# Performance work log

Measured on AMD Instinct MI355X. Metric: run time of the kernel, lower is better.

Reference implementation:

```python
import jax, jax.numpy as jnp
import numpy as np

N_NODES = 50000
N_EDGES = 800000
IN_FEATS = 256
OUT_FEATS = 32
NUM_HEADS = 8
NEG_SLOPE = 0.2


def setup_inputs() -> dict:
    key = jax.random.key(0)
    k_feat, k_src, k_dst, k_w, k_al, k_ar = jax.random.split(key, 6)
    feat = jax.random.normal(k_feat, (N_NODES, IN_FEATS), dtype=jnp.float32)
    src = jax.random.randint(k_src, (N_EDGES,), 0, N_NODES)
    dst = jax.random.randint(k_dst, (N_EDGES,), 0, N_NODES)
    # fc weight, stored as [in, H*F] so projection is feat @ W
    W = jax.random.normal(k_w, (IN_FEATS, NUM_HEADS * OUT_FEATS), dtype=jnp.float32) * 0.05
    attn_l = jax.random.normal(k_al, (NUM_HEADS, OUT_FEATS), dtype=jnp.float32) * 0.1
    attn_r = jax.random.normal(k_ar, (NUM_HEADS, OUT_FEATS), dtype=jnp.float32) * 0.1
    bias = jnp.zeros((NUM_HEADS, OUT_FEATS), dtype=jnp.float32)
    return {"feat": feat, "W": W, "attn_l": attn_l, "attn_r": attn_r,
            "bias": bias, "src": src, "dst": dst}


def reference(feat, W, attn_l, attn_r, bias, src, dst):
    N = feat.shape[0]
    H, F = attn_l.shape
    # node projection: [N, H, F]
    h = (feat @ W).reshape(N, H, F)
    # per-node attention logits (source code uses feat_src for both el and er)
    el = jnp.einsum('nhf,hf->nh', h, attn_l)  # [N, H]
    er = jnp.einsum('nhf,hf->nh', h, attn_r)  # [N, H]
    # per-edge logit: u_add_v then LeakyReLU
    e = el[src] + er[dst]                      # [E, H]
    e = jnp.where(e > 0, e, NEG_SLOPE * e)
    # edge softmax normalized over incoming edges of each dst node
    m = jax.ops.segment_max(e, dst, num_segments=N)   # [N, H], -inf for 0-deg
    ex = jnp.exp(e - m[dst])                           # [E, H]
    s = jax.ops.segment_sum(ex, dst, num_segments=N)   # [N, H]
    a = ex / s[dst]                                     # [E, H]
    # weighted scatter-sum aggregation: u_mul_e -> sum
    msg = h[src] * a[:, :, None]                        # [E, H, F]
    rst = jax.ops.segment_sum(msg, dst, num_segments=N)  # [N, H, F]
    rst = rst + bias[None, :, :]
    return rst
```

## Files before the change

kernel.cpp:

```cpp
#include <hip/hip_runtime.h>
#include <math.h>

#define NN 50000
#define NE 800000
#define IN_F 256
#define HF 256
#define NH 8
#define NEG_SLOPE 0.2f
#define CAP 64

#define GEMM_BLOCKS 782
#define EDGE_BLOCKS 3125
#define ELR_BLOCKS 12500
#define AGG_BLOCKS 3125

typedef short bf16x8 __attribute__((ext_vector_type(8)));
typedef float f32x16 __attribute__((ext_vector_type(16)));

__device__ __forceinline__ unsigned short f2bf(float x) {
    unsigned u = __float_as_uint(x);
    u += 0x7FFF + ((u >> 16) & 1);
    return (unsigned short)(u >> 16);
}
__device__ __forceinline__ float bf2f(unsigned short b) {
    return __uint_as_float(((unsigned)b) << 16);
}

__global__ void fill2_kernel(const int* __restrict__ src, const int* __restrict__ dst,
                             int* __restrict__ cnt, int* __restrict__ slots) {
    int e = blockIdx.x * 256 + threadIdx.x;
    if (e < NE) {
        int d = dst[e];
        int pos = atomicAdd(&cnt[d], 1);
        if (pos < CAP) slots[(size_t)d * CAP + pos] = src[e];
    }
}

__global__ __launch_bounds__(256) void wconv_kernel(const float* __restrict__ W,
                                                    unsigned short* __restrict__ Wb) {
    int e = blockIdx.x * 256 + threadIdx.x;
    int k = e >> 8, n = e & 255;
    float x = W[e];
    int kt = k >> 5, kk = k & 31;
    Wb[((size_t)(kt * 256 + n)) * 32 + kk] = f2bf(x);
}

__global__ __launch_bounds__(256) void gemm_kernel(const float* __restrict__ feat,
                                                   const unsigned short* __restrict__ Wb,
                                                   unsigned short* __restrict__ h, int M) {
    __shared__ __align__(16) unsigned short As_hi[2][64][40];
    __shared__ __align__(16) unsigned short As_lo[2][64][40];

    const int tid = threadIdx.x;
    const int lane = tid & 63;
    const int wid = tid >> 6;
    const int bm = blockIdx.x * 64;

    const int arow = tid >> 2;
    const int achk = tid & 3;
    const int grow = bm + arow;
    const int crow = (grow < M) ? grow : 0;
    const float* ap = feat + (size_t)crow * IN_F + achk * 8;

    f32x16 acc[2][2];
    #pragma unroll
    for (int mi = 0; mi < 2; ++mi)
        #pragma unroll
        for (int ni = 0; ni < 2; ++ni)
            #pragma unroll
            for (int r = 0; r < 16; ++r) acc[mi][ni][r] = 0.f;

    const int khalf = lane >> 5;
    const int nbase = wid * 64 + (lane & 31);

    float4 cur0 = *(const float4*)(ap);
    float4 cur1 = *(const float4*)(ap + 4);

    for (int kt = 0; kt < 8; ++kt) {
        const int buf = kt & 1;
        float4 nxt0, nxt1;
        if (kt < 7) {
            nxt0 = *(const float4*)(ap + (kt + 1) * 32);
            nxt1 = *(const float4*)(ap + (kt + 1) * 32 + 4);
        }
        bf16x8 bh[2][2];
        #pragma unroll
        for (int ksc = 0; ksc < 2; ++ksc)
            #pragma unroll
            for (int ni = 0; ni < 2; ++ni)
                bh[ksc][ni] = *(const bf16x8*)(Wb
                    + ((size_t)(kt * 256) + nbase + ni * 32) * 32
                    + (ksc * 2 + khalf) * 8);

        float xs[8] = {cur0.x, cur0.y, cur0.z, cur0.w, cur1.x, cur1.y, cur1.z, cur1.w};
        unsigned hi2[4], lo2[4];
        #pragma unroll
        for (int p = 0; p < 4; ++p) {
            unsigned short h0 = f2bf(xs[2 * p]), h1 = f2bf(xs[2 * p + 1]);
            unsigned short l0 = f2bf(xs[2 * p] - bf2f(h0));
            unsigned short l1 = f2bf(xs[2 * p + 1] - bf2f(h1));
            hi2[p] = (unsigned)h0 | ((unsigned)h1 << 16);
            lo2[p] = (unsigned)l0 | ((unsigned)l1 << 16);
        }
        *(int4*)&As_hi[buf][arow][achk * 8] = make_int4(hi2[0], hi2[1], hi2[2], hi2[3]);
        *(int4*)&As_lo[buf][arow][achk * 8] = make_int4(lo2[0], lo2[1], lo2[2], lo2[3]);
        __syncthreads();

        #pragma unroll
        for (int ksc = 0; ksc < 2; ++ksc) {
            const int kchunk = ksc * 2 + khalf;
            bf16x8 ah[2], av[2];
            #pragma unroll
            for (int mi = 0; mi < 2; ++mi) {
                int r = mi * 32 + (lane & 31);
                ah[mi] = *(const bf16x8*)&As_hi[buf][r][kchunk * 8];
                av[mi] = *(const bf16x8*)&As_lo[buf][r][kchunk * 8];
            }
            #pragma unroll
            for (int mi = 0; mi < 2; ++mi)
                #pragma unroll
                for (int ni = 0; ni < 2; ++ni) {
                    acc[mi][ni] = __builtin_amdgcn_mfma_f32_32x32x16_bf16(ah[mi], bh[ksc][ni], acc[mi][ni], 0, 0, 0);
                    acc[mi][ni] = __builtin_amdgcn_mfma_f32_32x32x16_bf16(av[mi], bh[ksc][ni], acc[mi][ni], 0, 0, 0);
                }
        }
        cur0 = nxt0;
        cur1 = nxt1;
    }

    #pragma unroll
    for (int mi = 0; mi < 2; ++mi)
        #pragma unroll
        for (int ni = 0; ni < 2; ++ni)
            #pragma unroll
            for (int r = 0; r < 16; ++r) {
                int row = mi * 32 + (r & 3) + 8 * (r >> 2) + 4 * (lane >> 5);
                int col = wid * 64 + ni * 32 + (lane & 31);
                int gr = bm + row;
                if (gr < M) h[(size_t)gr * HF + col] = f2bf(acc[mi][ni][r]);
            }
}

__global__ __launch_bounds__(256) void elr_kernel(const unsigned short* __restrict__ h,
                                                  const float* __restrict__ al,
                                                  const float* __restrict__ ar,
                                                  float* __restrict__ el,
                                                  float* __restrict__ er) {
    int node = blockIdx.x * 4 + (threadIdx.x >> 6);
    if (node >= NN) return;
    int lane = threadIdx.x & 63;
    short4 hv = *(const short4*)&h[(size_t)node * HF + lane * 4];
    float h0 = bf2f((unsigned short)hv.x), h1 = bf2f((unsigned short)hv.y);
    float h2 = bf2f((unsigned short)hv.z), h3 = bf2f((unsigned short)hv.w);
    float4 alv = *(const float4*)&al[lane * 4];
    float4 arv = *(const float4*)&ar[lane * 4];
    float pl = h0 * alv.x + h1 * alv.y + h2 * alv.z + h3 * alv.w;
    float pr = h0 * arv.x + h1 * arv.y + h2 * arv.z + h3 * arv.w;
    #pragma unroll
    for (int off = 1; off < 8; off <<= 1) {
        pl += __shfl_xor(pl, off);
        pr += __shfl_xor(pr, off);
    }
    if ((lane & 7) == 0) {
        el[node * NH + (lane >> 3)] = pl;
        er[node * NH + (lane >> 3)] = pr;
    }
}

__global__ __launch_bounds__(256) void agg_kernel(const unsigned short* __restrict__ h,
                                                  const float* __restrict__ el,
                                                  const float* __restrict__ er,
                                                  const int* __restrict__ cnt,
                                                  const int* __restrict__ slots,
                                                  const float* __restrict__ bias,
                                                  float* __restrict__ out) {
    int wv = blockIdx.x * 4 + (threadIdx.x >> 6);
    int lane = threadIdx.x & 63;
    int eg = lane >> 3;
    int fg = lane & 7;
    int e2 = (lane >> 5) & 1, e1 = (lane >> 4) & 1, e0 = (lane >> 3) & 1;
    int col = fg * 32 + eg * 4;
    float4 bv = *(const float4*)&bias[col];

    #pragma unroll 1
    for (int t = 0; t < 4; ++t) {
        int node = wv * 4 + t;
        int deg = cnt[node];
        deg = deg < CAP ? deg : CAP;
        const int* sl = slots + (size_t)node * CAP;
        float er_mine = er[(size_t)node * NH + fg];

        float ssum = 0.f;
        float acc[32];
        #pragma unroll
        for (int j = 0; j < 32; ++j) acc[j] = 0.f;

        for (int i0 = 0; i0 < deg; i0 += 16) {
            int idxA = i0 + eg;
            int idxB = i0 + 8 + eg;
            bool vA = idxA < deg, vB = idxB < deg;
            int sA = sl[vA ? idxA : 0];
            int sB = sl[vB ? idxB : 0];
            float eA = el[(size_t)sA * NH + fg] + er_mine;
            float eB = el[(size_t)sB * NH + fg] + er_mine;
            eA = eA > 0.f ? eA : NEG_SLOPE * eA;
            eB = eB > 0.f ? eB : NEG_SLOPE * eB;
            float pA = vA ? __expf(eA) : 0.f;
            float pB = vB ? __expf(eB) : 0.f;
            ssum += pA + pB;
            const unsigned short* hpA = h + (size_t)sA * HF + fg * 32;
            const unsigned short* hpB = h + (size_t)sB * HF + fg * 32;
            bf16x8 va[4], vb[4];
            #pragma unroll
            for (int c = 0; c < 4; ++c) { va[c] = *(const bf16x8*)(hpA + c * 8); }
            #pragma unroll
            for (int c = 0; c < 4; ++c) { vb[c] = *(const bf16x8*)(hpB + c * 8); }
            #pragma unroll
            for (int c = 0; c < 4; ++c)
                #pragma unroll
                for (int k = 0; k < 8; ++k) {
                    acc[c * 8 + k] = fmaf(bf2f((unsigned short)va[c][k]), pA, acc[c * 8 + k]);
                    acc[c * 8 + k] = fmaf(bf2f((unsigned short)vb[c][k]), pB, acc[c * 8 + k]);
                }
        }

        ssum += __shfl_xor(ssum, 8);
        ssum += __shfl_xor(ssum, 16);
        ssum += __shfl_xor(ssum, 32);
        float inv_s = (ssum > 0.f) ? 1.f / ssum : 0.f;

        float t16[16];
        #pragma unroll
        for (int j = 0; j < 16; ++j) {
            float keep = e2 ? acc[16 + j] : acc[j];
            float send = e2 ? acc[j] : acc[16 + j];
            t16[j] = keep + __shfl_xor(send, 32);
        }
        float t8[8];
        #pragma unroll
        for (int j = 0; j < 8; ++j) {
            float keep = e1 ? t16[8 + j] : t16[j];
            float send = e1 ? t16[j] : t16[8 + j];
            t8[j] = keep + __shfl_xor(send, 16);
        }
        float t4[4];
        #pragma unroll
        for (int j = 0; j < 4; ++j) {
            float keep = e0 ? t8[4 + j] : t8[j];
            float send = e0 ? t8[j] : t8[4 + j];
            t4[j] = keep + __shfl_xor(send, 8);
        }

        float4 o = make_float4(fmaf(t4[0], inv_s, bv.x), fmaf(t4[1], inv_s, bv.y),
                               fmaf(t4[2], inv_s, bv.z), fmaf(t4[3], inv_s, bv.w));
        *(float4*)&out[(size_t)node * HF + col] = o;
    }
}

extern "C" void kernel_launch(void* const* d_in, const int* in_sizes, int n_in,
                              void* d_out, int out_size, void* d_ws, size_t ws_size,
                              hipStream_t stream) {
    const float* feat = (const float*)d_in[0];
    const float* W    = (const float*)d_in[1];
    const float* al   = (const float*)d_in[2];
    const float* ar   = (const float*)d_in[3];
    const float* bias = (const float*)d_in[4];
    const int*   src  = (const int*)d_in[5];
    const int*   dst  = (const int*)d_in[6];
    float* out = (float*)d_out;

    char* ws = (char*)d_ws;
    size_t off = 0;
    unsigned short* h = (unsigned short*)(ws + off); off += (size_t)NN * HF * 2;
    float* el = (float*)(ws + off);                  off += (size_t)NN * NH * 4;
    float* er = (float*)(ws + off);                  off += (size_t)NN * NH * 4;
    int* cnt = (int*)(ws + off);                     off += (size_t)NN * 4;
    int* slots = (int*)(ws + off);                   off += (size_t)NN * CAP * 4;
    unsigned short* Wb = (unsigned short*)(ws + off); off += (size_t)IN_F * HF * 2;

    hipMemsetAsync(cnt, 0, (size_t)NN * 4, stream);

    fill2_kernel<<<EDGE_BLOCKS, 256, 0, stream>>>(src, dst, cnt, slots);
    wconv_kernel<<<256, 256, 0, stream>>>(W, Wb);
    gemm_kernel<<<GEMM_BLOCKS, 256, 0, stream>>>(feat, Wb, h, NN);
    elr_kernel<<<ELR_BLOCKS, 256, 0, stream>>>(h, al, ar, el, er);
    agg_kernel<<<AGG_BLOCKS, 256, 0, stream>>>(h, el, er, cnt, slots, bias, out);
}
```

Baseline: 161.4 us.

## Fuse attention logit computation into aggregation and store edge slots as 16-bit

Removes the separate elr kernel and its el/er buffers. The aggregation kernel now computes er for each destination node from its own h row. It computes el for each source edge from the h row it already loads for the message, using attn_l held in registers. Adjacency slots are stored as 16-bit indices, which is valid because there are fewer than 65536 nodes, and the four node degrees are read with one vector load. The aim is to save a kernel launch and the el/er memory traffic, at the cost of redundant per-edge dot products and higher register pressure in the aggregation loop.

New measurement: 199.6 us, median of 2. +23.6%, slower.

```diff
diff --git a/kernel.cpp b/kernel.cpp
--- a/kernel.cpp
+++ b/kernel.cpp
@@ -11,7 +11,6 @@
 
 #define GEMM_BLOCKS 782
 #define EDGE_BLOCKS 3125
-#define ELR_BLOCKS 12500
 #define AGG_BLOCKS 3125
 
 typedef short bf16x8 __attribute__((ext_vector_type(8)));
@@ -27,12 +26,12 @@
 }
 
 __global__ void fill2_kernel(const int* __restrict__ src, const int* __restrict__ dst,
-                             int* __restrict__ cnt, int* __restrict__ slots) {
+                             int* __restrict__ cnt, unsigned short* __restrict__ slots) {
     int e = blockIdx.x * 256 + threadIdx.x;
     if (e < NE) {
         int d = dst[e];
         int pos = atomicAdd(&cnt[d], 1);
-        if (pos < CAP) slots[(size_t)d * CAP + pos] = src[e];
+        if (pos < CAP) slots[(size_t)d * CAP + pos] = (unsigned short)src[e];
     }
 }
 
@@ -141,37 +140,11 @@
             }
 }
 
-__global__ __launch_bounds__(256) void elr_kernel(const unsigned short* __restrict__ h,
+__global__ __launch_bounds__(256) void agg_kernel(const unsigned short* __restrict__ h,
                                                   const float* __restrict__ al,
                                                   const float* __restrict__ ar,
-                                                  float* __restrict__ el,
-                                                  float* __restrict__ er) {
-    int node = blockIdx.x * 4 + (threadIdx.x >> 6);
-    if (node >= NN) return;
-    int lane = threadIdx.x & 63;
-    short4 hv = *(const short4*)&h[(size_t)node * HF + lane * 4];
-    float h0 = bf2f((unsigned short)hv.x), h1 = bf2f((unsigned short)hv.y);
-    float h2 = bf2f((unsigned short)hv.z), h3 = bf2f((unsigned short)hv.w);
-    float4 alv = *(const float4*)&al[lane * 4];
-    float4 arv = *(const float4*)&ar[lane * 4];
-    float pl = h0 * alv.x + h1 * alv.y + h2 * alv.z + h3 * alv.w;
-    float pr = h0 * arv.x + h1 * arv.y + h2 * arv.z + h3 * arv.w;
-    #pragma unroll
-    for (int off = 1; off < 8; off <<= 1) {
-        pl += __shfl_xor(pl, off);
-        pr += __shfl_xor(pr, off);
-    }
-    if ((lane & 7) == 0) {
-        el[node * NH + (lane >> 3)] = pl;
-        er[node * NH + (lane >> 3)] = pr;
-    }
-}
-
-__global__ __launch_bounds__(256) void agg_kernel(const unsigned short* __restrict__ h,
-                                                  const float* __restrict__ el,
-                                                  const float* __restrict__ er,
                                                   const int* __restrict__ cnt,
-                                                  const int* __restrict__ slots,
+                                                  const unsigned short* __restrict__ slots,
                                                   const float* __restrict__ bias,
                                                   float* __restrict__ out) {
     int wv = blockIdx.x * 4 + (threadIdx.x >> 6);
@@ -182,13 +155,37 @@
     int col = fg * 32 + eg * 4;
     float4 bv = *(const float4*)&bias[col];
 
+    float alf[32];
+    #pragma unroll
+    for (int c = 0; c < 8; ++c) {
+        float4 v = *(const float4*)&al[fg * 32 + c * 4];
+        alf[c * 4 + 0] = v.x; alf[c * 4 + 1] = v.y;
+        alf[c * 4 + 2] = v.z; alf[c * 4 + 3] = v.w;
+    }
+
+    int4 deg4 = *(const int4*)&cnt[wv * 4];
+
     #pragma unroll 1
     for (int t = 0; t < 4; ++t) {
         int node = wv * 4 + t;
-        int deg = cnt[node];
+        int deg = (t == 0) ? deg4.x : (t == 1) ? deg4.y : (t == 2) ? deg4.z : deg4.w;
         deg = deg < CAP ? deg : CAP;
-        const int* sl = slots + (size_t)node * CAP;
-        float er_mine = er[(size_t)node * NH + fg];
+        const unsigned short* sl = slots + (size_t)node * CAP;
+
+        float er_mine = 0.f;
+        {
+            const unsigned short* hn = h + (size_t)node * HF + fg * 32;
+            #pragma unroll
+            for (int c = 0; c < 4; ++c) {
+                bf16x8 hv = *(const bf16x8*)(hn + c * 8);
+                float4 r0 = *(const float4*)&ar[fg * 32 + c * 8];
+                float4 r1 = *(const float4*)&ar[fg * 32 + c * 8 + 4];
+                er_mine += bf2f((unsigned short)hv[0]) * r0.x + bf2f((unsigned short)hv[1]) * r0.y
+                         + bf2f((unsigned short)hv[2]) * r0.z + bf2f((unsigned short)hv[3]) * r0.w
+                         + bf2f((unsigned short)hv[4]) * r1.x + bf2f((unsigned short)hv[5]) * r1.y
+                         + bf2f((unsigned short)hv[6]) * r1.z + bf2f((unsigned short)hv[7]) * r1.w;
+            }
+        }
 
         float ssum = 0.f;
         float acc[32];
@@ -201,20 +198,30 @@
             bool vA = idxA < deg, vB = idxB < deg;
             int sA = sl[vA ? idxA : 0];
             int sB = sl[vB ? idxB : 0];
-            float eA = el[(size_t)sA * NH + fg] + er_mine;
-            float eB = el[(size_t)sB * NH + fg] + er_mine;
+            const unsigned short* hpA = h + (size_t)sA * HF + fg * 32;
+            const unsigned short* hpB = h + (size_t)sB * HF + fg * 32;
+            bf16x8 va[4], vb[4];
+            #pragma unroll
+            for (int c = 0; c < 4; ++c) { va[c] = *(const bf16x8*)(hpA + c * 8); }
+            #pragma unroll
+            for (int c = 0; c < 4; ++c) { vb[c] = *(const bf16x8*)(hpB + c * 8); }
+
+            float elA = 0.f, elB = 0.f;
+            #pragma unroll
+            for (int c = 0; c < 4; ++c)
+                #pragma unroll
+                for (int k = 0; k < 8; ++k) {
+                    elA = fmaf(bf2f((unsigned short)va[c][k]), alf[c * 8 + k], elA);
+                    elB = fmaf(bf2f((unsigned short)vb[c][k]), alf[c * 8 + k], elB);
+                }
+            float eA = elA + er_mine;
+            float eB = elB + er_mine;
             eA = eA > 0.f ? eA : NEG_SLOPE * eA;
             eB = eB > 0.f ? eB : NEG_SLOPE * eB;
             float pA = vA ? __expf(eA) : 0.f;
             float pB = vB ? __expf(eB) : 0.f;
             ssum += pA + pB;
-            const unsigned short* hpA = h + (size_t)sA * HF + fg * 32;
-            const unsigned short* hpB = h + (size_t)sB * HF + fg * 32;
-            bf16x8 va[4], vb[4];
-            #pragma unroll
-            for (int c = 0; c < 4; ++c) { va[c] = *(const bf16x8*)(hpA + c * 8); }
-            #pragma unroll
-            for (int c = 0; c < 4; ++c) { vb[c] = *(const bf16x8*)(hpB + c * 8); }
+
             #pragma unroll
             for (int c = 0; c < 4; ++c)
                 #pragma unroll
@@ -271,18 +278,15 @@
 
     char* ws = (char*)d_ws;
     size_t off = 0;
-    unsigned short* h = (unsigned short*)(ws + off); off += (size_t)NN * HF * 2;
-    float* el = (float*)(ws + off);                  off += (size_t)NN * NH * 4;
-    float* er = (float*)(ws + off);                  off += (size_t)NN * NH * 4;
-    int* cnt = (int*)(ws + off);                     off += (size_t)NN * 4;
-    int* slots = (int*)(ws + off);                   off += (size_t)NN * CAP * 4;
-    unsigned short* Wb = (unsigned short*)(ws + off); off += (size_t)IN_F * HF * 2;
+    unsigned short* h = (unsigned short*)(ws + off);     off += (size_t)NN * HF * 2;
+    int* cnt = (int*)(ws + off);                         off += (size_t)NN * 4;
+    unsigned short* slots = (unsigned short*)(ws + off); off += (size_t)NN * CAP * 2;
+    unsigned short* Wb = (unsigned short*)(ws + off);    off += (size_t)IN_F * HF * 2;
 
     hipMemsetAsync(cnt, 0, (size_t)NN * 4, stream);
 
     fill2_kernel<<<EDGE_BLOCKS, 256, 0, stream>>>(src, dst, cnt, slots);
     wconv_kernel<<<256, 256, 0, stream>>>(W, Wb);
     gemm_kernel<<<GEMM_BLOCKS, 256, 0, stream>>>(feat, Wb, h, NN);
-    elr_kernel<<<ELR_BLOCKS, 256, 0, stream>>>(h, al, ar, el, er);
-    agg_kernel<<<AGG_BLOCKS, 256, 0, stream>>>(h, el, er, cnt, slots, bias, out);
-}
+    agg_kernel<<<AGG_BLOCKS, 256, 0, stream>>>(h, al, ar, cnt, slots, bias, out);
+}
```
